# Kernel optimization log

Hardware: AMD Instinct MI355X
Metric: run time of the kernel (lower is better)

## Reference

```python
import jax, jax.numpy as jnp
import numpy as np

B, S, E, H = 8, 1024, 1024, 16
D = E // H  # head_dim = hidden_size // num_heads


def setup_inputs() -> dict:
    key = jax.random.key(0)
    ks = jax.random.split(key, 9)
    s = 0.02
    return {
        "h":  jax.random.normal(ks[0], (B, S, E), jnp.float32),
        # per-head projection weights stacked over heads; torch Linear(E, D) -> stored [E, D] (x @ W)
        "Wq": jax.random.normal(ks[1], (H, E, D), jnp.float32) * s,
        "bq": jax.random.normal(ks[2], (H, D), jnp.float32) * s,
        "Wk": jax.random.normal(ks[3], (H, E, D), jnp.float32) * s,
        "bk": jax.random.normal(ks[4], (H, D), jnp.float32) * s,
        "Wv": jax.random.normal(ks[5], (H, E, D), jnp.float32) * s,  # dead weight: original passes h as value
        "bv": jax.random.normal(ks[6], (H, D), jnp.float32) * s,
        "Wo": jax.random.normal(ks[7], (E, E), jnp.float32) * s,
        "bo": jax.random.normal(ks[8], (E,), jnp.float32) * s,
    }


def reference(h, Wq, bq, Wk, bk, Wv, bv, Wo, bo):
    # Batched over all heads at once instead of the original Python loop.
    q = jnp.einsum('bse,hed->bhsd', h, Wq) + bq[None, :, None, :]   # [B,H,S,D]
    k = jnp.einsum('bse,hed->bhsd', h, Wk) + bk[None, :, None, :]   # [B,H,S,D]
    # v is computed in the original module but NOT used (do_attention gets h as value)
    _v = jnp.einsum('bse,hed->bhsd', h, Wv) + bv[None, :, None, :]
    scale = 1.0 / jnp.sqrt(jnp.asarray(D, h.dtype))
    scores = jnp.einsum('bhsd,bhtd->bhst', q, k) * scale            # [B,H,S,T]
    # original: F.softmax(scores, dim=1) on per-head [B,S,T] -> query axis = axis 2 here
    weights = jax.nn.softmax(scores, axis=2)
    ctx = jnp.einsum('bhst,bte->bhse', weights, h)                  # value = h (embed_dim), per original
    # torch.cat over dim=1 of per-head [B,S,E] outputs -> [B, H*S, E]
    x = ctx.reshape(B, H * S, E)
    return x @ Wo + bo
```

## Files before the change

### kernel.cpp

```cpp
#include <hip/hip_runtime.h>

#define B_ 8
#define S_ 1024
#define E_ 1024
#define H_ 16
#define D_ 64

typedef __attribute__((ext_vector_type(8))) __bf16 bf16x8;
typedef __attribute__((ext_vector_type(4))) float f32x4;
typedef __attribute__((ext_vector_type(4))) unsigned short u16x4;
typedef __attribute__((ext_vector_type(8))) unsigned short u16x8;

static __device__ __forceinline__ unsigned short f2bf_hw(float f) {
  union { __bf16 b; unsigned short u; } v;
  v.b = (__bf16)f;
  return v.u;
}

#if __has_builtin(__builtin_amdgcn_exp2f)
#define EXP2(x) __builtin_amdgcn_exp2f(x)
#else
#define EXP2(x) exp2f(x)
#endif
#define SCALE2 0.18033688f

#define MFMA16(a, b, c) __builtin_amdgcn_mfma_f32_16x16x32_bf16((a), (b), (c), 0, 0, 0)

__global__ void cast_f32_bf16_kernel(const float* __restrict__ src,
                                     unsigned short* __restrict__ dst, int n4) {
  int i = blockIdx.x * 256 + threadIdx.x;
  if (i >= n4) return;
  float4 v = reinterpret_cast<const float4*>(src)[i];
  u16x4 o;
  o[0] = f2bf_hw(v.x); o[1] = f2bf_hw(v.y); o[2] = f2bf_hw(v.z); o[3] = f2bf_hw(v.w);
  reinterpret_cast<u16x4*>(dst)[i] = o;
}

__global__ void transpose_cast_kernel(const float* __restrict__ src,
                                      unsigned short* __restrict__ dst,
                                      int rows, int cols) {
  __shared__ unsigned short tile[64][65];
  const float* s = src + (size_t)blockIdx.z * rows * cols;
  unsigned short* d = dst + (size_t)blockIdx.z * rows * cols;
  int rb = blockIdx.y * 64, cb = blockIdx.x * 64;
#pragma unroll
  for (int k = 0; k < 16; k++) {
    int idx = threadIdx.x + 256 * k;
    int r = idx >> 6, c = idx & 63;
    tile[r][c] = f2bf_hw(s[(size_t)(rb + r) * cols + cb + c]);
  }
  __syncthreads();
#pragma unroll
  for (int k = 0; k < 16; k++) {
    int idx = threadIdx.x + 256 * k;
    int r = idx >> 6, c = idx & 63;
    d[(size_t)(cb + r) * rows + rb + c] = tile[c][r];
  }
}

__launch_bounds__(256)
__global__ void gemm_G_kernel(const unsigned short* __restrict__ hb,
                              const unsigned short* __restrict__ WoT,
                              unsigned short* __restrict__ Gt) {
  int mblk = blockIdx.x, nblk = blockIdx.y, b = blockIdx.z;
  const unsigned short* A = hb + (size_t)b * S_ * E_;
  int tid = threadIdx.x, l = tid & 63, w = tid >> 6;
  int ws = w & 1, wc = w >> 1, lr = l & 15, lg = l >> 4;
  f32x4 acc[4][4] = {};
  int ar[4], bc[4];
#pragma unroll
  for (int i = 0; i < 4; i++) ar[i] = mblk * 128 + ws * 64 + i * 16 + lr;
#pragma unroll
  for (int j = 0; j < 4; j++) bc[j] = nblk * 128 + wc * 64 + j * 16 + lr;
  for (int k0 = 0; k0 < E_; k0 += 32) {
    bf16x8 a[4], bb[4];
#pragma unroll
    for (int i = 0; i < 4; i++)
      a[i] = *reinterpret_cast<const bf16x8*>(A + (size_t)ar[i] * E_ + k0 + lg * 8);
#pragma unroll
    for (int j = 0; j < 4; j++)
      bb[j] = *reinterpret_cast<const bf16x8*>(WoT + (size_t)bc[j] * E_ + k0 + lg * 8);
#pragma unroll
    for (int i = 0; i < 4; i++)
#pragma unroll
      for (int j = 0; j < 4; j++)
        acc[i][j] = MFMA16(a[i], bb[j], acc[i][j]);
  }
#pragma unroll
  for (int i = 0; i < 4; i++) {
    int t0 = mblk * 128 + ws * 64 + i * 16 + lg * 4;
#pragma unroll
    for (int j = 0; j < 4; j++) {
      u16x4 p;
#pragma unroll
      for (int r = 0; r < 4; r++) p[r] = f2bf_hw(acc[i][j][r]);
      int e = bc[j];
      size_t addr = (((size_t)b * 4 + (e >> 8)) * 32 + (t0 >> 5)) * 8192 +
                    (size_t)(e & 255) * 32 + (t0 & 31);
      *reinterpret_cast<u16x4*>(Gt + addr) = p;
    }
  }
}

__launch_bounds__(256)
__global__ void proj_qk_kernel(const unsigned short* __restrict__ hb,
                               const unsigned short* __restrict__ WqT,
                               const unsigned short* __restrict__ WkT,
                               const float* __restrict__ bq,
                               const float* __restrict__ bk,
                               unsigned short* __restrict__ Qb,
                               unsigned short* __restrict__ Kb) {
  int sblk = blockIdx.x, z = blockIdx.y;
  int b = z >> 4, h = z & 15;
  const unsigned short* A = hb + (size_t)b * S_ * E_;
  const unsigned short* Btq = WqT + (size_t)h * D_ * E_;
  const unsigned short* Btk = WkT + (size_t)h * D_ * E_;
  int tid = threadIdx.x, l = tid & 63, w = tid >> 6;
  int ws = w & 1, wc = w >> 1, lr = l & 15, lg = l >> 4;
  f32x4 accq[4][2] = {}, acck[4][2] = {};
  int ar[4], bc[2];
#pragma unroll
  for (int i = 0; i < 4; i++) ar[i] = sblk * 128 + ws * 64 + i * 16 + lr;
#pragma unroll
  for (int j = 0; j < 2; j++) bc[j] = wc * 32 + j * 16 + lr;
  for (int k0 = 0; k0 < E_; k0 += 32) {
    bf16x8 a[4], bbq[2], bbk[2];
#pragma unroll
    for (int i = 0; i < 4; i++)
      a[i] = *reinterpret_cast<const bf16x8*>(A + (size_t)ar[i] * E_ + k0 + lg * 8);
#pragma unroll
    for (int j = 0; j < 2; j++) {
      bbq[j] = *reinterpret_cast<const bf16x8*>(Btq + (size_t)bc[j] * E_ + k0 + lg * 8);
      bbk[j] = *reinterpret_cast<const bf16x8*>(Btk + (size_t)bc[j] * E_ + k0 + lg * 8);
    }
#pragma unroll
    for (int i = 0; i < 4; i++)
#pragma unroll
      for (int j = 0; j < 2; j++) {
        accq[i][j] = MFMA16(a[i], bbq[j], accq[i][j]);
        acck[i][j] = MFMA16(a[i], bbk[j], acck[i][j]);
      }
  }
  unsigned short* oq = Qb + (size_t)z * S_ * D_;
  unsigned short* ok = Kb + (size_t)z * S_ * D_;
#pragma unroll
  for (int j = 0; j < 2; j++) {
    float bvq = bq[h * D_ + bc[j]], bvk = bk[h * D_ + bc[j]];
#pragma unroll
    for (int i = 0; i < 4; i++)
#pragma unroll
      for (int r = 0; r < 4; r++) {
        int s = sblk * 128 + ws * 64 + i * 16 + lg * 4 + r;
        oq[(size_t)s * D_ + bc[j]] = f2bf_hw(accq[i][j][r] + bvq);
        ok[(size_t)s * D_ + bc[j]] = f2bf_hw(acck[i][j][r] + bvk);
      }
  }
}

__launch_bounds__(256)
__global__ void stats_kernel(const unsigned short* __restrict__ Qb,
                             const unsigned short* __restrict__ Kb,
                             float* __restrict__ c) {
  int tblk = blockIdx.x, z = blockIdx.y;
  const unsigned short* Q = Qb + (size_t)z * S_ * D_;
  const unsigned short* K = Kb + (size_t)z * S_ * D_;
  int tid = threadIdx.x, l = tid & 63, w = tid >> 6;
  int lr = l & 15, lg = l >> 4;
  int tb = tblk * 256 + w * 64;
  const float scale = 0.125f;
  bf16x8 kb[4][2];
#pragma unroll
  for (int j = 0; j < 4; j++)
#pragma unroll
    for (int ks = 0; ks < 2; ks++)
      kb[j][ks] = *reinterpret_cast<const bf16x8*>(
          K + (size_t)(tb + j * 16 + lr) * D_ + ks * 32 + lg * 8);
  float m[4], zz[4];
#pragma unroll
  for (int j = 0; j < 4; j++) { m[j] = -1e30f; zz[j] = 0.f; }
  for (int s0 = 0; s0 < S_; s0 += 32) {
    bf16x8 aq[2][2];
#pragma unroll
    for (int sf = 0; sf < 2; sf++)
#pragma unroll
      for (int ks = 0; ks < 2; ks++)
        aq[sf][ks] = *reinterpret_cast<const bf16x8*>(
            Q + (size_t)(s0 + sf * 16 + lr) * D_ + ks * 32 + lg * 8);
    f32x4 acc[2][4] = {};
#pragma unroll
    for (int sf = 0; sf < 2; sf++)
#pragma unroll
      for (int j = 0; j < 4; j++) {
        acc[sf][j] = MFMA16(aq[sf][0], kb[j][0], acc[sf][j]);
        acc[sf][j] = MFMA16(aq[sf][1], kb[j][1], acc[sf][j]);
      }
#pragma unroll
    for (int j = 0; j < 4; j++) {
      float v[8];
#pragma unroll
      for (int sf = 0; sf < 2; sf++)
#pragma unroll
        for (int r = 0; r < 4; r++) v[sf * 4 + r] = acc[sf][j][r] * scale;
      float mx = m[j];
#pragma unroll
      for (int t = 0; t < 8; t++) mx = fmaxf(mx, v[t]);
      float sum = 0.f;
#pragma unroll
      for (int t = 0; t < 8; t++) sum += __expf(v[t] - mx);
      zz[j] = zz[j] * __expf(m[j] - mx) + sum;
      m[j] = mx;
    }
  }
#pragma unroll
  for (int j = 0; j < 4; j++) {
    float mj = m[j], zj = zz[j];
#pragma unroll
    for (int off = 16; off <= 32; off <<= 1) {
      float om = __shfl_xor(mj, off, 64);
      float oz = __shfl_xor(zj, off, 64);
      float mn = fmaxf(mj, om);
      zj = zj * __expf(mj - mn) + oz * __expf(om - mn);
      mj = mn;
    }
    if (l < 16)
      c[(size_t)z * S_ + tb + j * 16 + lr] = (mj + __logf(zj)) * 1.44269504f;
  }
}

__launch_bounds__(256, 3)
__global__ void attn_kernel(const unsigned short* __restrict__ Qb,
                            const unsigned short* __restrict__ Kb,
                            const unsigned short* __restrict__ Gt,
                            const float* __restrict__ cst,
                            const float* __restrict__ bo,
                            float* __restrict__ out) {
  int n = blockIdx.x;
  int b = n & 7, h = (n >> 3) & 15, eblk = (n >> 7) & 3, sblk = n >> 9;
  int z = b * 16 + h;
  __shared__ unsigned short Ks[2][32][72];
  __shared__ unsigned short Ps[64][40];
  int tid = threadIdx.x, l = tid & 63, w = tid >> 6;
  int lr = l & 15, lg = l >> 4;
  const unsigned short* Q = Qb + (size_t)z * S_ * D_ + (size_t)(sblk * 64) * D_;
  const unsigned short* K = Kb + (size_t)z * S_ * D_;
  const unsigned short* Gb = Gt + (((size_t)b * 4 + eblk) * 32) * 8192;
  const float* cz = cst + (size_t)z * S_;

  bf16x8 q[2];
#pragma unroll
  for (int ks = 0; ks < 2; ks++)
    q[ks] = *reinterpret_cast<const bf16x8*>(
        Q + (size_t)(w * 16 + lr) * D_ + ks * 32 + lg * 8);

  size_t goff[4];
#pragma unroll
  for (int j = 0; j < 4; j++)
    goff[j] = (size_t)(w * 64 + j * 16 + lr) * 32 + lg * 8;

  int krow = tid >> 3, kc8 = (tid & 7) * 8;
  u16x8 kreg;
  bf16x8 vA[4], vB[4];

  kreg = *reinterpret_cast<const u16x8*>(K + (size_t)krow * D_ + kc8);
  *reinterpret_cast<u16x8*>(&Ks[0][krow][kc8]) = kreg;
  kreg = *reinterpret_cast<const u16x8*>(K + (size_t)(32 + krow) * D_ + kc8);
#pragma unroll
  for (int j = 0; j < 4; j++)
    vA[j] = *reinterpret_cast<const bf16x8*>(Gb + goff[j]);
  __syncthreads();

  f32x4 acc[4][4] = {};

#define WINDOW(IT, CUR, VCUR, VNXT)                                               \
  do {                                                                            \
    int t0_ = (IT) * 32;                                                          \
                            \
    *reinterpret_cast<u16x8*>(&Ks[(CUR) ^ 1][krow][kc8]) = kreg;                  \
    {                                                                             \
      int tk_ = ((IT) + 2) & 31;                                                  \
      kreg = *reinterpret_cast<const u16x8*>(                                     \
          K + (size_t)(tk_ * 32 + krow) * D_ + kc8);                              \
    }                                                                             \
                       \
    {                                                                             \
      int tg_ = ((IT) + 1) & 31;                                                  \
      _Pragma("unroll") for (int j = 0; j < 4; j++)                               \
        VNXT[j] = *reinterpret_cast<const bf16x8*>(                               \
            Gb + (size_t)tg_ * 8192 + goff[j]);                                   \
    }                                                                             \
                        \
    {                                                                             \
      bf16x8 ka_[2][2];                                                           \
      _Pragma("unroll") for (int tf = 0; tf < 2; tf++)                            \
        _Pragma("unroll") for (int ks = 0; ks < 2; ks++)                          \
          ka_[tf][ks] = *reinterpret_cast<const bf16x8*>(                         \
              &Ks[CUR][tf * 16 + lr][ks * 32 + lg * 8]);                          \
      f32x4 sa_[2] = {};                                                          \
      _Pragma("unroll") for (int tf = 0; tf < 2; tf++) {                          \
        sa_[tf] = MFMA16(ka_[tf][0], q[0], sa_[tf]);                              \
        sa_[tf] = MFMA16(ka_[tf][1], q[1], sa_[tf]);                              \
      }                                                                           \
      _Pragma("unroll") for (int tf = 0; tf < 2; tf++) {                          \
        f32x4 cv_ = *reinterpret_cast<const f32x4*>(cz + t0_ + tf * 16 + lg * 4); \
        u16x4 p_;                                                                 \
        _Pragma("unroll") for (int r = 0; r < 4; r++)                             \
          p_[r] = f2bf_hw(EXP2(fmaf(sa_[tf][r], SCALE2, -cv_[r])));               \
        *reinterpret_cast<u16x4*>(&Ps[w * 16 + lr][tf * 16 + lg * 4]) = p_;       \
      }                                                                           \
    }                                                                             \
    __syncthreads();                                                \
                  \
    {                                                                             \
      bf16x8 ap_[4];                                                              \
      _Pragma("unroll") for (int i = 0; i < 4; i++)                               \
        ap_[i] = *reinterpret_cast<const bf16x8*>(&Ps[i * 16 + lr][lg * 8]);      \
      __builtin_amdgcn_s_setprio(1);                                              \
      _Pragma("unroll") for (int i = 0; i < 4; i++)                               \
        _Pragma("unroll") for (int j = 0; j < 4; j++)                             \
          acc[i][j] = MFMA16(ap_[i], VCUR[j], acc[i][j]);                         \
      __builtin_amdgcn_s_setprio(0);                                              \
    }                                                                             \
    __syncthreads();                                        \
  } while (0)

  for (int it2 = 0; it2 < 16; ++it2) {
    WINDOW(it2 * 2, 0, vA, vB);
    WINDOW(it2 * 2 + 1, 1, vB, vA);
  }
#undef WINDOW

  float bov[4];
#pragma unroll
  for (int j = 0; j < 4; j++) bov[j] = bo[eblk * 256 + w * 64 + j * 16 + lr];
#pragma unroll
  for (int i = 0; i < 4; i++)
#pragma unroll
    for (int j = 0; j < 4; j++)
#pragma unroll
      for (int r = 0; r < 4; r++) {
        int s = sblk * 64 + i * 16 + lg * 4 + r;
        int col = eblk * 256 + w * 64 + j * 16 + lr;
        out[((size_t)b * (H_ * S_) + (size_t)h * S_ + s) * E_ + col] =
            acc[i][j][r] + bov[j];
      }
}

extern "C" void kernel_launch(void* const* d_in, const int* in_sizes, int n_in,
                              void* d_out, int out_size, void* d_ws, size_t ws_size,
                              hipStream_t stream) {
  const float* h  = (const float*)d_in[0];
  const float* Wq = (const float*)d_in[1];
  const float* bq = (const float*)d_in[2];
  const float* Wk = (const float*)d_in[3];
  const float* bk = (const float*)d_in[4];
  const float* Wo = (const float*)d_in[7];
  const float* bo = (const float*)d_in[8];
  float* out = (float*)d_out;

  char* p = (char*)d_ws;
  unsigned short* hb  = (unsigned short*)p; p += (size_t)B_ * S_ * E_ * 2;
  unsigned short* WoT = (unsigned short*)p; p += (size_t)E_ * E_ * 2;
  unsigned short* WqT = (unsigned short*)p; p += (size_t)H_ * D_ * E_ * 2;
  unsigned short* WkT = (unsigned short*)p; p += (size_t)H_ * D_ * E_ * 2;
  unsigned short* Qb  = (unsigned short*)p; p += (size_t)B_ * H_ * S_ * D_ * 2;
  unsigned short* Kb  = (unsigned short*)p; p += (size_t)B_ * H_ * S_ * D_ * 2;
  unsigned short* Gt  = (unsigned short*)p; p += (size_t)B_ * E_ * S_ * 2;
  float*          cst = (float*)p;          p += (size_t)B_ * H_ * S_ * 4;

  int n4 = B_ * S_ * E_ / 4;
  cast_f32_bf16_kernel<<<dim3(n4 / 256), 256, 0, stream>>>(h, hb, n4);
  transpose_cast_kernel<<<dim3(16, 16, 1), 256, 0, stream>>>(Wo, WoT, E_, E_);
  transpose_cast_kernel<<<dim3(1, 16, H_), 256, 0, stream>>>(Wq, WqT, E_, D_);
  transpose_cast_kernel<<<dim3(1, 16, H_), 256, 0, stream>>>(Wk, WkT, E_, D_);
  gemm_G_kernel<<<dim3(8, 8, B_), 256, 0, stream>>>(hb, WoT, Gt);
  proj_qk_kernel<<<dim3(8, B_ * H_), 256, 0, stream>>>(hb, WqT, WkT, bq, bk, Qb, Kb);
  stats_kernel<<<dim3(S_ / 256, B_ * H_), 256, 0, stream>>>(Qb, Kb, cst);
  attn_kernel<<<dim3(8192), 256, 0, stream>>>(Qb, Kb, Gt, cst, bo, out);
}
```

Measured before the change: 632.0 us.

## Software-pipeline attention window: overlap P·V of previous tile with QK of current

Double-buffers the probability tile in shared memory and restructures each window so the P·V MFMAs for the previous key tile run alongside the QK MFMAs and exp of the current tile. This removes one __syncthreads per window and lets the matrix and transcendental work interleave instead of serializing. In exchange the kernel uses more LDS, changes the register lifetime of the V fragments, and needs an epilogue step for the last tile.

```diff
diff --git a/kernel.cpp b/kernel.cpp
--- a/kernel.cpp
+++ b/kernel.cpp
@@ -238,7 +238,7 @@
   int b = n & 7, h = (n >> 3) & 15, eblk = (n >> 7) & 3, sblk = n >> 9;
   int z = b * 16 + h;
   __shared__ unsigned short Ks[2][32][72];
-  __shared__ unsigned short Ps[64][40];
+  __shared__ unsigned short Ps[2][64][40];
   int tid = threadIdx.x, l = tid & 63, w = tid >> 6;
   int lr = l & 15, lg = l >> 4;
   const unsigned short* Q = Qb + (size_t)z * S_ * D_ + (size_t)(sblk * 64) * D_;
@@ -271,7 +271,7 @@
 
   f32x4 acc[4][4] = {};
 
-#define WINDOW(IT, CUR, VCUR, VNXT)                                               \
+#define WINDOW(IT, CUR, VPREV, HASPV)                                             \
   do {                                                                            \
     int t0_ = (IT) * 32;                                                          \
                             \
@@ -281,53 +281,66 @@
       kreg = *reinterpret_cast<const u16x8*>(                                     \
           K + (size_t)(tk_ * 32 + krow) * D_ + kc8);                              \
     }                                                                             \
-                       \
-    {                                                                             \
-      int tg_ = ((IT) + 1) & 31;                                                  \
-      _Pragma("unroll") for (int j = 0; j < 4; j++)                               \
-        VNXT[j] = *reinterpret_cast<const bf16x8*>(                               \
-            Gb + (size_t)tg_ * 8192 + goff[j]);                                   \
-    }                                                                             \
-                        \
+                                                         \
+    f32x4 sa_[2] = {};                                                            \
     {                                                                             \
       bf16x8 ka_[2][2];                                                           \
       _Pragma("unroll") for (int tf = 0; tf < 2; tf++)                            \
         _Pragma("unroll") for (int ks = 0; ks < 2; ks++)                          \
           ka_[tf][ks] = *reinterpret_cast<const bf16x8*>(                         \
               &Ks[CUR][tf * 16 + lr][ks * 32 + lg * 8]);                          \
-      f32x4 sa_[2] = {};                                                          \
       _Pragma("unroll") for (int tf = 0; tf < 2; tf++) {                          \
         sa_[tf] = MFMA16(ka_[tf][0], q[0], sa_[tf]);                              \
         sa_[tf] = MFMA16(ka_[tf][1], q[1], sa_[tf]);                              \
       }                                                                           \
-      _Pragma("unroll") for (int tf = 0; tf < 2; tf++) {                          \
-        f32x4 cv_ = *reinterpret_cast<const f32x4*>(cz + t0_ + tf * 16 + lg * 4); \
-        u16x4 p_;                                                                 \
-        _Pragma("unroll") for (int r = 0; r < 4; r++)                             \
-          p_[r] = f2bf_hw(EXP2(fmaf(sa_[tf][r], SCALE2, -cv_[r])));               \
-        *reinterpret_cast<u16x4*>(&Ps[w * 16 + lr][tf * 16 + lg * 4]) = p_;       \
-      }                                                                           \
-    }                                                                             \
-    __syncthreads();                                                \
-                  \
-    {                                                                             \
+    }                                                                             \
+                 \
+    if (HASPV) {                                                                  \
       bf16x8 ap_[4];                                                              \
       _Pragma("unroll") for (int i = 0; i < 4; i++)                               \
-        ap_[i] = *reinterpret_cast<const bf16x8*>(&Ps[i * 16 + lr][lg * 8]);      \
+        ap_[i] = *reinterpret_cast<const bf16x8*>(                                \
+            &Ps[(CUR) ^ 1][i * 16 + lr][lg * 8]);                                 \
       __builtin_amdgcn_s_setprio(1);                                              \
       _Pragma("unroll") for (int i = 0; i < 4; i++)                               \
         _Pragma("unroll") for (int j = 0; j < 4; j++)                             \
-          acc[i][j] = MFMA16(ap_[i], VCUR[j], acc[i][j]);                         \
+          acc[i][j] = MFMA16(ap_[i], VPREV[j], acc[i][j]);                        \
       __builtin_amdgcn_s_setprio(0);                                              \
     }                                                                             \
-    __syncthreads();                                        \
+           \
+    {                                                                             \
+      int tg_ = ((IT) + 1) & 31;                                                  \
+      _Pragma("unroll") for (int j = 0; j < 4; j++)                               \
+        VPREV[j] = *reinterpret_cast<const bf16x8*>(                              \
+            Gb + (size_t)tg_ * 8192 + goff[j]);                                   \
+    }                                                                             \
+                                                         \
+    _Pragma("unroll") for (int tf = 0; tf < 2; tf++) {                            \
+      f32x4 cv_ = *reinterpret_cast<const f32x4*>(cz + t0_ + tf * 16 + lg * 4);   \
+      u16x4 p_;                                                                   \
+      _Pragma("unroll") for (int r = 0; r < 4; r++)                               \
+        p_[r] = f2bf_hw(EXP2(fmaf(sa_[tf][r], SCALE2, -cv_[r])));                 \
+      *reinterpret_cast<u16x4*>(&Ps[CUR][w * 16 + lr][tf * 16 + lg * 4]) = p_;    \
+    }                                                                             \
+    __syncthreads();                                                              \
   } while (0)
 
   for (int it2 = 0; it2 < 16; ++it2) {
-    WINDOW(it2 * 2, 0, vA, vB);
-    WINDOW(it2 * 2 + 1, 1, vB, vA);
+    WINDOW(it2 * 2, 0, vB, (it2 > 0));
+    WINDOW(it2 * 2 + 1, 1, vA, true);
   }
 #undef WINDOW
+
+  {
+    bf16x8 ap_[4];
+#pragma unroll
+    for (int i = 0; i < 4; i++)
+      ap_[i] = *reinterpret_cast<const bf16x8*>(&Ps[1][i * 16 + lr][lg * 8]);
+#pragma unroll
+    for (int i = 0; i < 4; i++)
+#pragma unroll
+      for (int j = 0; j < 4; j++)
+        acc[i][j] = MFMA16(ap_[i], vB[j], acc[i][j]);
+  }
 
   float bov[4];
 #pragma unroll
```

After: 645.4 us. +2.1%, slower.
